# Kernel tuning notes

Hardware: AMD Instinct MI355X
Metric: run time of the kernel (lower is better)

The kernel has to match this reference:

```python
import jax, jax.numpy as jnp
import numpy as np

K = 256
D = 64
N = 262144


def setup_inputs() -> dict:
    key = jax.random.key(0)
    k1, k2, k3 = jax.random.split(key, 3)
    X = jax.random.normal(k1, (N, D), dtype=jnp.float32)
    mu = jax.random.uniform(k2, (K, D), dtype=jnp.float32)
    logvar = jax.random.uniform(k3, (K,), dtype=jnp.float32)
    alpha = jnp.full((K,), np.float32(np.log(1.0 / K)), dtype=jnp.float32)
    return {"X": X, "mu": mu, "logvar": logvar, "alpha": alpha}


def reference(X, mu, logvar, alpha):
    # Squared L2 distance via ||x||^2 + ||mu||^2 - 2 mu.x  (avoids (K,N,D) intermediate)
    x2 = jnp.sum(X * X, axis=1)          # (N,)
    m2 = jnp.sum(mu * mu, axis=1)        # (K,)
    cross = jnp.einsum('kd,nd->kn', mu, X)  # (K,N)
    a = m2[:, None] + x2[None, :] - 2.0 * cross  # (K,N) squared distances
    b = jnp.exp(logvar)[:, None]                 # (K,1) variances
    return alpha[:, None] - 0.5 * D * logvar[:, None] - 0.5 * (a / b)
```

## Files before the change

### kernel.cpp

```cpp
#include <hip/hip_runtime.h>
#include <hip/hip_bf16.h>

typedef _Float16 half8 __attribute__((ext_vector_type(8)));
typedef float f32x16 __attribute__((ext_vector_type(16)));

constexpr int KC = 256;
constexpr int DD = 64;
constexpr int NN = 262144;
constexpr int GRID = 1024;


__global__ __launch_bounds__(512, 8)
void gmm_ll_kernel(const float* __restrict__ X,
                   const float* __restrict__ mu,
                   const float* __restrict__ logvar,
                   const float* __restrict__ alpha,
                   float* __restrict__ out)
{
    __shared__ __align__(16) unsigned char smu[KC * 128];
    __shared__ float2 AC[KC];

    const int tid = threadIdx.x;

    if (tid < KC) {
        const float* mrow = mu + tid * DD;
        float m2 = 0.f;
        #pragma unroll
        for (int s = 0; s < 8; ++s) {
            float4 v0 = *(const float4*)(mrow + 8 * s);
            float4 v1 = *(const float4*)(mrow + 8 * s + 4);
            m2 += v0.x*v0.x + v0.y*v0.y + v0.z*v0.z + v0.w*v0.w
                + v1.x*v1.x + v1.y*v1.y + v1.z*v1.z + v1.w*v1.w;
            half8 hch = { (_Float16)v0.x, (_Float16)v0.y, (_Float16)v0.z, (_Float16)v0.w,
                          (_Float16)v1.x, (_Float16)v1.y, (_Float16)v1.z, (_Float16)v1.w };
            *(half8*)(smu + tid * 128 + ((s ^ (tid & 7)) * 16)) = hch;
        }
        float lv = logvar[tid];
        float Cv = __expf(-lv);
        AC[tid] = make_float2(alpha[tid] - 32.0f * lv - 0.5f * m2 * Cv, Cv);
    }
    __syncthreads();

    const int l = tid & 63;
    const int w = tid >> 6;
    const int q = l & 31;
    const int h = l >> 5;

    const int col = blockIdx.x * 256 + w * 32 + q;
    const float* xr = X + (size_t)col * DD;

    half8 bf[4];
    float p = 0.f;
    #pragma unroll
    for (int kk = 0; kk < 4; ++kk) {
        float4 v0 = *(const float4*)(xr + kk * 16 + h * 8);
        float4 v1 = *(const float4*)(xr + kk * 16 + h * 8 + 4);
        p += v0.x*v0.x + v0.y*v0.y + v0.z*v0.z + v0.w*v0.w
           + v1.x*v1.x + v1.y*v1.y + v1.z*v1.z + v1.w*v1.w;
        bf[kk] = { (_Float16)v0.x, (_Float16)v0.y, (_Float16)v0.z, (_Float16)v0.w,
                   (_Float16)v1.x, (_Float16)v1.y, (_Float16)v1.z, (_Float16)v1.w };
    }
    p += __shfl_xor(p, 32, 64);
    const float hx2 = 0.5f * p;

    #pragma unroll 2
    for (int c = 0; c < 8; ++c) {
        f32x16 acc = {0.f,0.f,0.f,0.f,0.f,0.f,0.f,0.f,
                      0.f,0.f,0.f,0.f,0.f,0.f,0.f,0.f};
        const int r = 32 * c + q;
        const unsigned rbase = (unsigned)r * 128u;
        const unsigned sw = (unsigned)(q & 7);
        #pragma unroll
        for (int kk = 0; kk < 4; ++kk) {
            half8 af = *(const half8*)(smu + rbase + ((((unsigned)(2*kk + h)) ^ sw) * 16));
            acc = __builtin_amdgcn_mfma_f32_32x32x16_f16(af, bf[kk], acc, 0, 0, 0);
        }
        #pragma unroll
        for (int g = 0; g < 4; ++g) {
            const int Rb = 32 * c + 8 * g + 4 * h;
            #pragma unroll
            for (int j = 0; j < 4; ++j) {
                const float2 ac = AC[Rb + j];
                out[(size_t)(Rb + j) * NN + col] = ac.x + (acc[4 * g + j] - hx2) * ac.y;
            }
        }
    }
}

extern "C" void kernel_launch(void* const* d_in, const int* in_sizes, int n_in,
                              void* d_out, int out_size, void* d_ws, size_t ws_size,
                              hipStream_t stream)
{
    const float* X  = (const float*)d_in[0];
    const float* mu = (const float*)d_in[1];
    const float* lv = (const float*)d_in[2];
    const float* al = (const float*)d_in[3];
    float* out = (float*)d_out;
    gmm_ll_kernel<<<GRID, 512, 0, stream>>>(X, mu, lv, al, out);
}
```

Before: 79.43 us.

## Process four column chunks per block to amortize mu staging and reuse A fragments

Each block now handles four 256-column chunks instead of one, and the grid shrinks from 1024 to 256 blocks. The shared-memory mu conversion and per-component constants are done once per four chunks, and each A fragment read from LDS is reused across four MFMAs. Block indices are remapped in a strided pattern, and the X loads are issued before the barrier so they overlap the mu staging. In exchange each thread holds more registers (launch bounds lowered to 2 blocks per CU) and there are fewer blocks, which may reduce latency hiding for this output-write-bound kernel.

```diff
diff --git a/kernel.cpp b/kernel.cpp
--- a/kernel.cpp
+++ b/kernel.cpp
@@ -7,10 +7,11 @@
 constexpr int KC = 256;
 constexpr int DD = 64;
 constexpr int NN = 262144;
-constexpr int GRID = 1024;
+constexpr int GRID = 256;
+constexpr int NCH = 4;
 
 
-__global__ __launch_bounds__(512, 8)
+__global__ __launch_bounds__(512, 2)
 void gmm_ll_kernel(const float* __restrict__ X,
                    const float* __restrict__ mu,
                    const float* __restrict__ logvar,
@@ -39,49 +40,65 @@
         float Cv = __expf(-lv);
         AC[tid] = make_float2(alpha[tid] - 32.0f * lv - 0.5f * m2 * Cv, Cv);
     }
-    __syncthreads();
 
     const int l = tid & 63;
     const int w = tid >> 6;
     const int q = l & 31;
     const int h = l >> 5;
 
-    const int col = blockIdx.x * 256 + w * 32 + q;
-    const float* xr = X + (size_t)col * DD;
+    const int b  = blockIdx.x;
+    const int bs = (b & 7) * (GRID / 8) + (b >> 3);
+    const int col0 = bs * (NCH * 256) + w * 32 + q;
 
-    half8 bf[4];
-    float p = 0.f;
+    half8 bf[NCH][4];
+    float hx2[NCH];
     #pragma unroll
-    for (int kk = 0; kk < 4; ++kk) {
-        float4 v0 = *(const float4*)(xr + kk * 16 + h * 8);
-        float4 v1 = *(const float4*)(xr + kk * 16 + h * 8 + 4);
-        p += v0.x*v0.x + v0.y*v0.y + v0.z*v0.z + v0.w*v0.w
-           + v1.x*v1.x + v1.y*v1.y + v1.z*v1.z + v1.w*v1.w;
-        bf[kk] = { (_Float16)v0.x, (_Float16)v0.y, (_Float16)v0.z, (_Float16)v0.w,
-                   (_Float16)v1.x, (_Float16)v1.y, (_Float16)v1.z, (_Float16)v1.w };
-    }
-    p += __shfl_xor(p, 32, 64);
-    const float hx2 = 0.5f * p;
-
-    #pragma unroll 2
-    for (int c = 0; c < 8; ++c) {
-        f32x16 acc = {0.f,0.f,0.f,0.f,0.f,0.f,0.f,0.f,
-                      0.f,0.f,0.f,0.f,0.f,0.f,0.f,0.f};
-        const int r = 32 * c + q;
-        const unsigned rbase = (unsigned)r * 128u;
-        const unsigned sw = (unsigned)(q & 7);
+    for (int ch = 0; ch < NCH; ++ch) {
+        const float* xr = X + (size_t)(col0 + ch * 256) * DD;
+        float p = 0.f;
         #pragma unroll
         for (int kk = 0; kk < 4; ++kk) {
-            half8 af = *(const half8*)(smu + rbase + ((((unsigned)(2*kk + h)) ^ sw) * 16));
-            acc = __builtin_amdgcn_mfma_f32_32x32x16_f16(af, bf[kk], acc, 0, 0, 0);
+            float4 v0 = *(const float4*)(xr + kk * 16 + h * 8);
+            float4 v1 = *(const float4*)(xr + kk * 16 + h * 8 + 4);
+            p += v0.x*v0.x + v0.y*v0.y + v0.z*v0.z + v0.w*v0.w
+               + v1.x*v1.x + v1.y*v1.y + v1.z*v1.z + v1.w*v1.w;
+            bf[ch][kk] = { (_Float16)v0.x, (_Float16)v0.y, (_Float16)v0.z, (_Float16)v0.w,
+                           (_Float16)v1.x, (_Float16)v1.y, (_Float16)v1.z, (_Float16)v1.w };
         }
+        p += __shfl_xor(p, 32, 64);
+        hx2[ch] = 0.5f * p;
+    }
+    __syncthreads();
+
+    #pragma unroll 1
+    for (int c = 0; c < 8; ++c) {
+        const unsigned rbase = (unsigned)(32 * c + q) * 128u;
+        const unsigned sw = (unsigned)(q & 7);
+        half8 af[4];
+        #pragma unroll
+        for (int kk = 0; kk < 4; ++kk)
+            af[kk] = *(const half8*)(smu + rbase + ((((unsigned)(2 * kk + h)) ^ sw) * 16));
+
+        f32x16 acc[NCH];
+        #pragma unroll
+        for (int ch = 0; ch < NCH; ++ch) {
+            acc[ch] = (f32x16){0.f,0.f,0.f,0.f,0.f,0.f,0.f,0.f,
+                               0.f,0.f,0.f,0.f,0.f,0.f,0.f,0.f};
+            #pragma unroll
+            for (int kk = 0; kk < 4; ++kk)
+                acc[ch] = __builtin_amdgcn_mfma_f32_32x32x16_f16(af[kk], bf[ch][kk], acc[ch], 0, 0, 0);
+        }
+
         #pragma unroll
         for (int g = 0; g < 4; ++g) {
             const int Rb = 32 * c + 8 * g + 4 * h;
             #pragma unroll
             for (int j = 0; j < 4; ++j) {
                 const float2 ac = AC[Rb + j];
-                out[(size_t)(Rb + j) * NN + col] = ac.x + (acc[4 * g + j] - hx2) * ac.y;
+                float* po = out + (size_t)(Rb + j) * NN + col0;
+                #pragma unroll
+                for (int ch = 0; ch < NCH; ++ch)
+                    po[ch * 256] = ac.x + (acc[ch][4 * g + j] - hx2[ch]) * ac.y;
             }
         }
     }
```

Result: faster. 73.19 us (-7.8%).
